# Optimization experiments

Measured on AMD Instinct MI355X. Metric: run time of the kernel, lower is better.

## Reference

```python
import jax, jax.numpy as jnp
import numpy as np


def _conv(x, w, pad):
    return jax.lax.conv_general_dilated(x, w, (1, 1), [(pad, pad), (pad, pad)],
                                        dimension_numbers=('NCHW', 'OIHW', 'NCHW'))


def _cbs(x, w, s, b, pad):
    # Conv + (folded inference BatchNorm as per-channel affine) + SiLU
    y = _conv(x, w, pad) * s[None, :, None, None] + b[None, :, None, None]
    return y * jax.nn.sigmoid(y)


def _pixel_shuffle(x, r):
    N, C, H, W = x.shape
    c = C // (r * r)
    return x.reshape(N, c, r, r, H, W).transpose(0, 1, 4, 2, 5, 3).reshape(N, c, H * r, W * r)


def _pixel_unshuffle(x, r):
    N, C, H, W = x.shape
    h, w = H // r, W // r
    return x.reshape(N, C, h, r, w, r).transpose(0, 1, 3, 5, 2, 4).reshape(N, C * r * r, h, w)


def _carafe(x, dw, db, ew, eb, k, up):
    # Content-aware reassembly: predict per-pixel k*k kernels for up*up sub-positions,
    # softmax-normalize, then gather-multiply-accumulate over k*k neighborhoods.
    N, C, H, W = x.shape
    kt = _conv(x, dw, 0) + db[None, :, None, None]
    if k % 2 == 0:
        kt = jnp.pad(kt, ((0, 0), (0, 0), (k // 2, k // 2 - 1), (k // 2, k // 2 - 1)))
        kt = _conv(kt, ew, 0) + eb[None, :, None, None]
    else:
        kt = _conv(kt, ew, k // 2) + eb[None, :, None, None]
    kt = _pixel_shuffle(kt, up)                     # [N, k*k, H*up, W*up]
    kt = jax.nn.softmax(kt, axis=1)
    # non-overlapping unfold(step=up) -> [N, H, W, k*k, up*up]
    kt = kt.reshape(N, k * k, H, up, W, up).transpose(0, 2, 4, 1, 3, 5).reshape(N, H, W, k * k, up * up)
    if k % 2 == 0:
        xp = jnp.pad(x, ((0, 0), (0, 0), (k // 2, k // 2 - 1), (k // 2, k // 2 - 1)))
    else:
        xp = jnp.pad(x, ((0, 0), (0, 0), (k // 2, k // 2), (k // 2, k // 2)))
    # k*k sliding patches (k is a small static constant)
    patches = jnp.stack([xp[:, :, i:i + H, j:j + W] for i in range(k) for j in range(k)], axis=-1)
    patches = patches.transpose(0, 2, 3, 1, 4)      # [N, H, W, C, k*k]
    out = jnp.einsum('nhwck,nhwkr->nhwcr', patches, kt)  # [N, H, W, C, up*up]
    out = out.reshape(N, H, W, C * up * up).transpose(0, 3, 1, 2)
    return _pixel_shuffle(out, up)


def _forward(x, cv1_w, cv1_s, cv1_b, m1a_w, m1a_s, m1a_b, m1b_w, m1b_s, m1b_b,
             cvm2_w, cvm2_s, cvm2_b, u2_down_w, u2_down_b, u2_enc_w, u2_enc_b,
             m2a_w, m2a_s, m2a_b, m2b_w, m2b_s, m2b_b,
             cvm3_w, cvm3_s, cvm3_b, u3_down_w, u3_down_b, u3_enc_w, u3_enc_b,
             m3a_w, m3a_s, m3a_b, m3b_w, m3b_s, m3b_b, cv2_w, cv2_s, cv2_b):
    C = cv1_w.shape[0] // 2
    t = _cbs(x, cv1_w, cv1_s, cv1_b, 0)
    y, y0 = t[:, :C], t[:, C:]

    def bneck(z, wa, sa, ba, wb, sb, bb):  # shortcut=False, e=1.0
        return _cbs(_cbs(z, wa, sa, ba, 1), wb, sb, bb, 1)

    y1 = bneck(y0, m1a_w, m1a_s, m1a_b, m1b_w, m1b_s, m1b_b)
    y2 = _cbs(_pixel_unshuffle(y1, 2), cvm2_w, cvm2_s, cvm2_b, 0)
    y2 = _carafe(y2, u2_down_w, u2_down_b, u2_enc_w, u2_enc_b, 1, 2) + y1
    y2 = bneck(y2, m2a_w, m2a_s, m2a_b, m2b_w, m2b_s, m2b_b)
    y3 = _cbs(_pixel_unshuffle(y2, 4), cvm3_w, cvm3_s, cvm3_b, 0)
    y3 = _carafe(y3, u3_down_w, u3_down_b, u3_enc_w, u3_enc_b, 2, 4) + y2
    y3 = bneck(y3, m3a_w, m3a_s, m3a_b, m3b_w, m3b_s, m3b_b)
    return _cbs(jnp.concatenate([y, y0, y1, y2, y3], axis=1), cv2_w, cv2_s, cv2_b, 0)


def setup_inputs() -> dict:
    key = jax.random.key(0)
    ks = jax.random.split(key, 16)
    C = 128

    def cbs_p(k, co, ci, ksz):
        k1, k2, k3 = jax.random.split(k, 3)
        w = jax.random.normal(k1, (co, ci, ksz, ksz), jnp.float32) / np.sqrt(ci * ksz * ksz).astype(np.float32)
        s = 1.0 + 0.1 * jax.random.normal(k2, (co,), jnp.float32)
        b = 0.1 * jax.random.normal(k3, (co,), jnp.float32)
        return w, s, b

    d = {}
    d['x'] = jax.random.normal(ks[0], (8, 256, 128, 128), jnp.float32)
    d['cv1_w'], d['cv1_s'], d['cv1_b'] = cbs_p(ks[1], 2 * C, 256, 1)
    for name, kk in (('m1', ks[2]), ('m2', ks[3]), ('m3', ks[4])):
        ka, kb = jax.random.split(kk)
        d[name + 'a_w'], d[name + 'a_s'], d[name + 'a_b'] = cbs_p(ka, C, C, 3)
        d[name + 'b_w'], d[name + 'b_s'], d[name + 'b_b'] = cbs_p(kb, C, C, 3)
    d['cvm2_w'], d['cvm2_s'], d['cvm2_b'] = cbs_p(ks[5], C, 4 * C, 1)
    d['cvm3_w'], d['cvm3_s'], d['cvm3_b'] = cbs_p(ks[6], C, 16 * C, 1)
    d['u2_down_w'] = jax.random.normal(ks[7], (C // 4, C, 1, 1), jnp.float32) / np.sqrt(C).astype(np.float32)
    d['u2_down_b'] = 0.1 * jax.random.normal(ks[8], (C // 4,), jnp.float32)
    d['u2_enc_w'] = jax.random.normal(ks[9], (4, C // 4, 1, 1), jnp.float32) / np.sqrt(C // 4).astype(np.float32)
    d['u2_enc_b'] = 0.1 * jax.random.normal(ks[10], (4,), jnp.float32)
    d['u3_down_w'] = jax.random.normal(ks[11], (C // 4, C, 1, 1), jnp.float32) / np.sqrt(C).astype(np.float32)
    d['u3_down_b'] = 0.1 * jax.random.normal(ks[12], (C // 4,), jnp.float32)
    d['u3_enc_w'] = jax.random.normal(ks[13], (64, C // 4, 2, 2), jnp.float32) / np.sqrt((C // 4) * 4).astype(np.float32)
    d['u3_enc_b'] = 0.1 * jax.random.normal(ks[14], (64,), jnp.float32)
    d['cv2_w'], d['cv2_s'], d['cv2_b'] = cbs_p(ks[15], 256, 5 * C, 1)
    return d


def reference(x, cv1_w, cv1_s, cv1_b, m1a_w, m1a_s, m1a_b, m1b_w, m1b_s, m1b_b,
              cvm2_w, cvm2_s, cvm2_b, u2_down_w, u2_down_b, u2_enc_w, u2_enc_b,
              m2a_w, m2a_s, m2a_b, m2b_w, m2b_s, m2b_b,
              cvm3_w, cvm3_s, cvm3_b, u3_down_w, u3_down_b, u3_enc_w, u3_enc_b,
              m3a_w, m3a_s, m3a_b, m3b_w, m3b_s, m3b_b, cv2_w, cv2_s, cv2_b):
    return _forward(x, cv1_w, cv1_s, cv1_b, m1a_w, m1a_s, m1a_b, m1b_w, m1b_s, m1b_b,
                    cvm2_w, cvm2_s, cvm2_b, u2_down_w, u2_down_b, u2_enc_w, u2_enc_b,
                    m2a_w, m2a_s, m2a_b, m2b_w, m2b_s, m2b_b,
                    cvm3_w, cvm3_s, cvm3_b, u3_down_w, u3_down_b, u3_enc_w, u3_enc_b,
                    m3a_w, m3a_s, m3a_b, m3b_w, m3b_s, m3b_b, cv2_w, cv2_s, cv2_b)
```

## Files before the change

### kernel.cpp

```cpp
#include <hip/hip_runtime.h>

typedef unsigned short u16;
typedef short v8s __attribute__((ext_vector_type(8)));
typedef u16 v8u __attribute__((ext_vector_type(8)));
typedef float v4f __attribute__((ext_vector_type(4)));
typedef __bf16 v8bf __attribute__((ext_vector_type(8)));

__device__ __forceinline__ float bf2f(u16 u) {
    unsigned x = ((unsigned)u) << 16; float f; __builtin_memcpy(&f, &x, 4); return f;
}
__device__ __forceinline__ u16 f2bf(float f) {
    unsigned x; __builtin_memcpy(&x, &f, 4);
    x = x + 0x7FFFu + ((x >> 16) & 1u);
    return (u16)(x >> 16);
}
__device__ __forceinline__ float silu(float v) { return v / (1.f + __expf(-v)); }

__device__ __forceinline__ void gld16(const void* g, void* l) {
    __builtin_amdgcn_global_load_lds(
        (const __attribute__((address_space(1))) unsigned int*)(uintptr_t)g,
        (__attribute__((address_space(3))) unsigned int*)(unsigned int)(uintptr_t)l,
        16, 0, 0);
}

__global__ void cvtw(const float* __restrict__ in, u16* __restrict__ out, int n) {
    int i = blockIdx.x * 256 + threadIdx.x;
    if (i < n) out[i] = f2bf(in[i]);
}
__global__ void wtrans3(const float* __restrict__ in, u16* __restrict__ out) {
    int i = blockIdx.x * 256 + threadIdx.x;
    if (i >= 147456) return;
    int tap = i % 9; int rem = i / 9; int ci = rem & 127; int co = rem >> 7;
    out[((tap * 128 + co) << 7) + ci] = f2bf(in[i]);
}
__global__ void wtrans_ps(const float* __restrict__ in, u16* __restrict__ out, int R2) {
    int i = blockIdx.x * 256 + threadIdx.x;
    int tap = i % R2; int rem = i / R2; int c = rem & 127; int co = rem >> 7;
    out[((tap * 128 + co) << 7) + c] = f2bf(in[i]);
}

__global__ __launch_bounds__(256) void nchw2nhwc(const float* __restrict__ in, u16* __restrict__ out) {
    __shared__ u16 tile[64][72];
    const int n = blockIdx.z, c0 = blockIdx.y * 64, p0 = blockIdx.x * 64;
#pragma unroll
    for (int rep = 0; rep < 16; ++rep) {
        int idx = rep * 256 + threadIdx.x;
        int c = idx >> 6, p = idx & 63;
        tile[c][p] = f2bf(in[((size_t)(n * 256 + c0 + c)) * 16384 + p0 + p]);
    }
    __syncthreads();
#pragma unroll
    for (int rep = 0; rep < 16; ++rep) {
        int idx = rep * 256 + threadIdx.x;
        int p = idx >> 6, c = idx & 63;
        out[((size_t)n * 16384 + p0 + p) * 256 + c0 + c] = tile[c][p];
    }
}

__global__ __launch_bounds__(256, 2) void conv3_mfma(
    const u16* __restrict__ src, int c0, int srcC,
    const u16* __restrict__ wt,
    const float* __restrict__ scale, const float* __restrict__ bias,
    u16* __restrict__ out) {
    __shared__ __align__(16) char smem[49152];
    const int n = blockIdx.y;
    const int hraw = blockIdx.x;
    const int h = ((hraw & 7) << 4) | (hraw >> 3);
    const int tid = threadIdx.x;
    const int lane = tid & 63;
    const int wv = tid >> 6;
    const int r = lane & 15, q = lane >> 4;
    const int wr = wv >> 1, wc = wv & 1;

    v4f acc[4][4];
#pragma unroll
    for (int a = 0; a < 4; ++a)
#pragma unroll
        for (int b = 0; b < 4; ++b) acc[a][b] = (v4f){0.f, 0.f, 0.f, 0.f};

    const size_t rowstride = (size_t)128 * srcC;
    const u16* nbase = src + (size_t)n * 128 * rowstride + c0;

    auto stage = [&](int koff) {
#pragma unroll
        for (int j = 0; j < 12; ++j) {
            int t = wv * 12 + j;
            int kh = t >> 4;
            int hh = h + kh - 1;
            char* dst = smem + t * 1024;
            if ((unsigned)hh < 128u) {
                int px = ((t & 15) << 3) + (lane >> 3);
                int cb = (lane & 7) * 16;
                cb ^= (px & 7) << 4;
                const char* g = (const char*)(nbase + (size_t)hh * rowstride + koff)
                                + (size_t)px * srcC * 2 + cb;
                gld16(g, dst);
            } else {
                *(v8s*)(dst + lane * 16) = (v8s){0, 0, 0, 0, 0, 0, 0, 0};
            }
        }
    };

    auto loadB = [&](v8bf (&B)[12], int kh, int koff, int k0l) {
#pragma unroll
        for (int kw = 0; kw < 3; ++kw)
#pragma unroll
            for (int nt = 0; nt < 4; ++nt)
                B[kw * 4 + nt] = __builtin_bit_cast(v8bf, *(const v8s*)(
                    wt + (size_t)((kh * 3 + kw) * 128 + wc * 64 + nt * 16 + r) * 128
                       + koff + k0l + q * 8));
    };

    auto comp = [&](v8bf (&B)[12], int kh, int k0l) {
#pragma unroll
        for (int kw = 0; kw < 3; ++kw) {
            v8bf afr[4];
#pragma unroll
            for (int mt = 0; mt < 4; ++mt) {
                int p = wr * 64 + mt * 16 + r + kw - 1;
                bool vp = (unsigned)p < 128u;
                int pc = vp ? p : 0;
                int o = kh * 16384 + pc * 128 + k0l * 2 + q * 16;
                o ^= (pc & 7) << 4;
                v8s av = *(const v8s*)(smem + o);
                if (!vp) av = (v8s){0, 0, 0, 0, 0, 0, 0, 0};
                afr[mt] = __builtin_bit_cast(v8bf, av);
            }
#pragma unroll
            for (int mt = 0; mt < 4; ++mt)
#pragma unroll
                for (int nt = 0; nt < 4; ++nt)
                    acc[mt][nt] = __builtin_amdgcn_mfma_f32_16x16x32_bf16(
                        afr[mt], B[kw * 4 + nt], acc[mt][nt], 0, 0, 0);
        }
    };

#pragma unroll
    for (int hf = 0; hf < 2; ++hf) {
        const int koff = hf * 64;
        __syncthreads();
        stage(koff);
        __syncthreads();
#pragma unroll
        for (int k0l = 0; k0l < 64; k0l += 32) {
            v8bf bA[12], bB[12];
            loadB(bA, 0, koff, k0l);
            loadB(bB, 1, koff, k0l);
            comp(bA, 0, k0l);
            loadB(bA, 2, koff, k0l);
            comp(bB, 1, k0l);
            comp(bA, 2, k0l);
        }
    }

    __syncthreads();
    u16* ldsO = (u16*)smem;
#pragma unroll
    for (int nt = 0; nt < 4; ++nt) {
        int co = wc * 64 + nt * 16 + r;
        float s = scale[co], bi = bias[co];
#pragma unroll
        for (int mt = 0; mt < 4; ++mt) {
#pragma unroll
            for (int i = 0; i < 4; ++i) {
                int p = wr * 64 + mt * 16 + q * 4 + i;
                ldsO[p * 136 + co] = f2bf(silu(acc[mt][nt][i] * s + bi));
            }
        }
    }
    __syncthreads();
    const size_t obase = ((size_t)n * 128 + h) * 128;
#pragma unroll
    for (int rep = 0; rep < 8; ++rep) {
        int px = rep * 16 + (tid >> 4);
        int c8 = (tid & 15) * 8;
        *(v8u*)(out + (obase + px) * 128 + c8) = *(const v8u*)&ldsO[px * 136 + c8];
    }
}

__global__ __launch_bounds__(256) void conv1_mfma(
    const u16* __restrict__ src, int srcC,
    const u16* __restrict__ wt,
    const float* __restrict__ scale, const float* __restrict__ bias,
    u16* __restrict__ out, int Cout) {
    __shared__ __align__(16) char smem[34816];
    const int n = blockIdx.z, co0 = blockIdx.y * 128, px0 = blockIdx.x * 128;
    const int tid = threadIdx.x;
    const int lane = tid & 63, wv = tid >> 6;
    const int r = lane & 15, q = lane >> 4;
    const int wr = wv >> 1, wc = wv & 1;

    v4f acc[4][4];
#pragma unroll
    for (int a = 0; a < 4; ++a)
#pragma unroll
        for (int b = 0; b < 4; ++b) acc[a][b] = (v4f){0.f, 0.f, 0.f, 0.f};

    const u16* abase = src + ((size_t)n * 16384 + px0) * srcC;

    auto stage = [&](int buf, int k0) {
#pragma unroll
        for (int j = 0; j < 4; ++j) {
            int o = j * 4096 + tid * 16;
            int s2 = o ^ ((o >> 3) & 0x70);
            int px = s2 >> 7, cb = s2 & 127;
            gld16((const char*)(abase + (size_t)px * srcC + k0) + cb,
                  smem + buf * 16384 + j * 4096 + wv * 1024);
        }
    };
    auto loadB = [&](v8bf (&B)[2][4], int k0) {
        const u16* wrow = wt + (size_t)(co0 + wc * 64 + r) * srcC + k0 + q * 8;
#pragma unroll
        for (int s = 0; s < 2; ++s)
#pragma unroll
            for (int nt = 0; nt < 4; ++nt)
                B[s][nt] = __builtin_bit_cast(v8bf,
                    *(const v8s*)(wrow + s * 32 + (size_t)nt * 16 * srcC));
    };

    v8bf bcur[2][4], bnxt[2][4];
    loadB(bcur, 0);
    stage(0, 0);
    int buf = 0;
    for (int k0 = 0; k0 < srcC; k0 += 64, buf ^= 1) {
        __syncthreads();
        bool more = (k0 + 64 < srcC);
        if (more) {
            loadB(bnxt, k0 + 64);
            stage(buf ^ 1, k0 + 64);
        }
#pragma unroll
        for (int s = 0; s < 2; ++s) {
            v8bf afr[4];
#pragma unroll
            for (int mt = 0; mt < 4; ++mt) {
                int ba = buf * 16384 + (wr * 64 + mt * 16 + r) * 128 + s * 64 + q * 16;
                ba ^= (ba >> 3) & 0x70;
                afr[mt] = __builtin_bit_cast(v8bf, *(const v8s*)(smem + ba));
            }
#pragma unroll
            for (int mt = 0; mt < 4; ++mt)
#pragma unroll
                for (int nt = 0; nt < 4; ++nt)
                    acc[mt][nt] = __builtin_amdgcn_mfma_f32_16x16x32_bf16(
                        afr[mt], bcur[s][nt], acc[mt][nt], 0, 0, 0);
        }
        if (more) {
#pragma unroll
            for (int s = 0; s < 2; ++s)
#pragma unroll
                for (int nt = 0; nt < 4; ++nt) bcur[s][nt] = bnxt[s][nt];
        }
    }

    __syncthreads();
    u16* ldsO = (u16*)smem;
#pragma unroll
    for (int nt = 0; nt < 4; ++nt) {
        int co = co0 + wc * 64 + nt * 16 + r;
        float s = scale[co], bi = bias[co];
#pragma unroll
        for (int mt = 0; mt < 4; ++mt) {
#pragma unroll
            for (int i = 0; i < 4; ++i) {
                int p = wr * 64 + mt * 16 + q * 4 + i;
                ldsO[p * 136 + (wc * 64 + nt * 16 + r)] = f2bf(silu(acc[mt][nt][i] * s + bi));
            }
        }
    }
    __syncthreads();
#pragma unroll
    for (int rep = 0; rep < 8; ++rep) {
        int px = rep * 16 + (tid >> 4);
        int c8 = (tid & 15) * 8;
        *(v8u*)(out + ((size_t)n * 16384 + px0 + px) * Cout + co0 + c8) =
            *(const v8u*)&ldsO[px * 136 + c8];
    }
}

__global__ __launch_bounds__(256) void cat_mfma(
    const u16* __restrict__ s0, const u16* __restrict__ s1,
    const u16* __restrict__ s2, const u16* __restrict__ s3,
    const u16* __restrict__ wt,
    const float* __restrict__ scale, const float* __restrict__ bias,
    float* __restrict__ out) {
    __shared__ __align__(16) u16 lds[2][128][64];
    const int n = blockIdx.z, co0 = blockIdx.y * 128, px0 = blockIdx.x * 128;
    const int tid = threadIdx.x;
    const int lane = tid & 63, wv = tid >> 6;
    const int r = lane & 15, q = lane >> 4;
    const int wr = wv >> 1, wc = wv & 1;

    v4f acc[4][4];
#pragma unroll
    for (int a = 0; a < 4; ++a)
#pragma unroll
        for (int b = 0; b < 4; ++b) acc[a][b] = (v4f){0.f, 0.f, 0.f, 0.f};

    const u16* srcs[4] = {s0, s1, s2, s3};
    const int sCq[4] = {256, 128, 128, 128};
    const int kbq[4] = {0, 256, 384, 512};
    const int segs[10] = {0, 0, 0, 0, 1, 1, 2, 2, 3, 3};
    const int k0s[10] = {0, 64, 128, 192, 0, 64, 0, 64, 0, 64};

    auto stage = [&](int buf, int c) {
        int seg = segs[c]; int sc = sCq[seg]; int k0 = k0s[c];
        const u16* ab = srcs[seg] + ((size_t)n * 16384 + px0) * sc;
#pragma unroll
        for (int j = 0; j < 4; ++j) {
            int o = j * 4096 + tid * 16;
            int s2 = o ^ ((o >> 3) & 0x70);
            int px = s2 >> 7, cb = s2 & 127;
            gld16((const char*)(ab + (size_t)px * sc + k0) + cb,
                  (char*)&lds[buf][0][0] + j * 4096 + wv * 1024);
        }
    };
    auto loadB = [&](v8bf (&B)[2][4], int c) {
        const u16* wrow = wt + (size_t)(co0 + wc * 64 + r) * 640 + kbq[segs[c]] + k0s[c] + q * 8;
#pragma unroll
        for (int s = 0; s < 2; ++s)
#pragma unroll
            for (int nt = 0; nt < 4; ++nt)
                B[s][nt] = __builtin_bit_cast(v8bf,
                    *(const v8s*)(wrow + s * 32 + (size_t)nt * 16 * 640));
    };

    v8bf bcur[2][4], bnxt[2][4];
    loadB(bcur, 0);
    stage(0, 0);
    int buf = 0;
#pragma unroll
    for (int c = 0; c < 10; ++c, buf ^= 1) {
        __syncthreads();
        if (c < 9) {
            loadB(bnxt, c + 1);
            stage(buf ^ 1, c + 1);
        }
#pragma unroll
        for (int s = 0; s < 2; ++s) {
            v8bf afr[4];
#pragma unroll
            for (int mt = 0; mt < 4; ++mt) {
                int ba = (wr * 64 + mt * 16 + r) * 128 + s * 64 + q * 16;
                ba ^= (ba >> 3) & 0x70;
                afr[mt] = __builtin_bit_cast(v8bf,
                    *(const v8s*)((const char*)&lds[buf][0][0] + ba));
            }
#pragma unroll
            for (int mt = 0; mt < 4; ++mt)
#pragma unroll
                for (int nt = 0; nt < 4; ++nt)
                    acc[mt][nt] = __builtin_amdgcn_mfma_f32_16x16x32_bf16(
                        afr[mt], bcur[s][nt], acc[mt][nt], 0, 0, 0);
        }
        if (c < 9) {
#pragma unroll
            for (int s = 0; s < 2; ++s)
#pragma unroll
                for (int nt = 0; nt < 4; ++nt) bcur[s][nt] = bnxt[s][nt];
        }
    }

#pragma unroll
    for (int nt = 0; nt < 4; ++nt) {
        int co = co0 + wc * 64 + nt * 16 + r;
        float s = scale[co], bi = bias[co];
#pragma unroll
        for (int mt = 0; mt < 4; ++mt) {
            int p = px0 + wr * 64 + mt * 16 + q * 4;
            v4f o;
#pragma unroll
            for (int i = 0; i < 4; ++i) o[i] = silu(acc[mt][nt][i] * s + bi);
            *(v4f*)(out + (size_t)(n * 256 + co) * 16384 + p) = o;
        }
    }
}

template <int KH, int KW, int S, int PAD, int CIN>
__global__ __launch_bounds__(256) void conv_mfma(
    const u16* __restrict__ src, int c0, int srcC,
    const u16* __restrict__ wt,
    const float* __restrict__ scale, const float* __restrict__ bias,
    u16* __restrict__ out, int Hin, int Win, int Wout, int Cout) {
    const int n = blockIdx.z;
    const int co0 = blockIdx.y * 64;
    const int hw0 = blockIdx.x * 64;
    const int tid = threadIdx.x;
    const int lane = tid & 63, wv = tid >> 6;
    const int r = lane & 15, q = lane >> 4;
    const int wr = wv >> 1, wc = wv & 1;

    const int m0 = hw0 + wr * 32 + r;
    const int m1 = m0 + 16;
    const int h0 = m0 / Wout, w0 = m0 - h0 * Wout;
    const int h1 = m1 / Wout, w1 = m1 - h1 * Wout;

    v4f acc00 = {0.f, 0.f, 0.f, 0.f}, acc01 = {0.f, 0.f, 0.f, 0.f};
    v4f acc10 = {0.f, 0.f, 0.f, 0.f}, acc11 = {0.f, 0.f, 0.f, 0.f};

    const u16* b0base = wt + (size_t)(co0 + wc * 32 + r) * CIN + q * 8;
    const size_t wtap = (size_t)Cout * CIN;

    int tap = 0;
#pragma unroll
    for (int kh = 0; kh < KH; ++kh)
#pragma unroll
        for (int kw = 0; kw < KW; ++kw, ++tap) {
            int ih0 = h0 * S + kh - PAD, iw0 = w0 * S + kw - PAD;
            int ih1 = h1 * S + kh - PAD, iw1 = w1 * S + kw - PAD;
            bool v0 = ((unsigned)ih0 < (unsigned)Hin) & ((unsigned)iw0 < (unsigned)Win);
            bool v1 = ((unsigned)ih1 < (unsigned)Hin) & ((unsigned)iw1 < (unsigned)Win);
            int p0i = v0 ? (n * Hin + ih0) * Win + iw0 : 0;
            int p1i = v1 ? (n * Hin + ih1) * Win + iw1 : 0;
            const u16* a0 = src + (size_t)p0i * srcC + c0 + q * 8;
            const u16* a1 = src + (size_t)p1i * srcC + c0 + q * 8;
            const u16* b0 = b0base + (size_t)tap * wtap;
            const u16* b1 = b0 + (size_t)16 * CIN;
#pragma unroll
            for (int k = 0; k < CIN; k += 32) {
                v8s za = {0, 0, 0, 0, 0, 0, 0, 0};
                v8s a0s = za, a1s = za;
                if (v0) a0s = *(const v8s*)(a0 + k);
                if (v1) a1s = *(const v8s*)(a1 + k);
                v8s b0s = *(const v8s*)(b0 + k);
                v8s b1s = *(const v8s*)(b1 + k);
                v8bf af0 = __builtin_bit_cast(v8bf, a0s);
                v8bf af1 = __builtin_bit_cast(v8bf, a1s);
                v8bf bw0 = __builtin_bit_cast(v8bf, b0s);
                v8bf bw1 = __builtin_bit_cast(v8bf, b1s);
                acc00 = __builtin_amdgcn_mfma_f32_16x16x32_bf16(af0, bw0, acc00, 0, 0, 0);
                acc01 = __builtin_amdgcn_mfma_f32_16x16x32_bf16(af0, bw1, acc01, 0, 0, 0);
                acc10 = __builtin_amdgcn_mfma_f32_16x16x32_bf16(af1, bw0, acc10, 0, 0, 0);
                acc11 = __builtin_amdgcn_mfma_f32_16x16x32_bf16(af1, bw1, acc11, 0, 0, 0);
            }
        }

    const int HWo = gridDim.x * 64;
#pragma unroll
    for (int ct = 0; ct < 2; ++ct) {
        v4f av0 = ct ? acc01 : acc00;
        v4f av1 = ct ? acc11 : acc10;
        int co = co0 + wc * 32 + ct * 16 + r;
        float s = scale[co], bb = bias[co];
        int mb = hw0 + wr * 32 + q * 4;
#pragma unroll
        for (int i = 0; i < 4; ++i) {
            float x0 = av0[i] * s + bb;
            float x1 = av1[i] * s + bb;
            out[((size_t)n * HWo + mb + i) * Cout + co] = f2bf(silu(x0));
            out[((size_t)n * HWo + mb + 16 + i) * Cout + co] = f2bf(silu(x1));
        }
    }
}

__global__ __launch_bounds__(256) void k_upadd(const u16* __restrict__ y2a,
                                               const u16* __restrict__ y1,
                                               u16* __restrict__ out) {
    int t = blockIdx.x * 256 + threadIdx.x;
    int cg = t & 15; int pix = t >> 4;
    int n = pix >> 14; int p = pix & 16383; int ho = p >> 7; int wo = p & 127;
    const u16* a = y2a + ((size_t)((n * 64 + (ho >> 1)) * 64 + (wo >> 1))) * 128 + cg * 8;
    const u16* b = y1 + (size_t)pix * 128 + cg * 8;
    v8s av = *(const v8s*)a;
    v8s bv = *(const v8s*)b;
    v8u o;
#pragma unroll
    for (int e = 0; e < 8; ++e) o[e] = f2bf(bf2f((u16)av[e]) + bf2f((u16)bv[e]));
    *(v8u*)(out + (size_t)pix * 128 + cg * 8) = o;
}

__global__ __launch_bounds__(256) void k_u3down(const u16* __restrict__ y3a,
                                                const float* __restrict__ w,
                                                const float* __restrict__ b,
                                                float* __restrict__ ktA) {
    int t = blockIdx.x * 256 + threadIdx.x;
    int co = t & 31; int pix = t >> 5;
    const u16* xr = y3a + (size_t)pix * 128;
    const float* wr = w + (size_t)co * 128;
    float acc = b[co];
#pragma unroll 16
    for (int k = 0; k < 128; ++k) acc += bf2f(xr[k]) * wr[k];
    ktA[t] = acc;
}

__global__ __launch_bounds__(256) void k_u3enc(const float* __restrict__ ktA,
                                               const float* __restrict__ ew,
                                               const float* __restrict__ eb,
                                               float* __restrict__ wtsm) {
    int t = blockIdx.x * 256 + threadIdx.x;
    int r = t & 15; int pix = t >> 4;
    int n = pix >> 10; int hw = pix & 1023; int h = hw >> 5; int w = hw & 31;
    float v[4];
#pragma unroll
    for (int kk = 0; kk < 4; ++kk) {
        int co = kk * 16 + r;
        float acc = eb[co];
#pragma unroll
        for (int dh = 0; dh < 2; ++dh)
#pragma unroll
            for (int dw = 0; dw < 2; ++dw) {
                int hh = h - 1 + dh, ww = w - 1 + dw;
                if (hh < 0 || ww < 0) continue;
                const float* kp = ktA + ((size_t)((n * 32 + hh) * 32 + ww)) * 32;
                const float* wp = ew + (size_t)co * 128 + dh * 2 + dw;
                for (int ci = 0; ci < 32; ++ci) acc += kp[ci] * wp[ci * 4];
            }
        v[kk] = acc;
    }
    float mx = fmaxf(fmaxf(v[0], v[1]), fmaxf(v[2], v[3]));
    float e0 = __expf(v[0] - mx), e1 = __expf(v[1] - mx), e2 = __expf(v[2] - mx), e3 = __expf(v[3] - mx);
    float inv = 1.f / (e0 + e1 + e2 + e3);
    float* o = wtsm + (size_t)t * 4;
    o[0] = e0 * inv; o[1] = e1 * inv; o[2] = e2 * inv; o[3] = e3 * inv;
}

__global__ __launch_bounds__(256) void k_carafe(const u16* __restrict__ y3a,
                                                const float* __restrict__ wtsm,
                                                const u16* __restrict__ y2,
                                                u16* __restrict__ out) {
    int t = blockIdx.x * 256 + threadIdx.x;
    int cg = t & 15; int pix = t >> 4;
    int n = pix >> 14; int p = pix & 16383; int ho = p >> 7; int wo = p & 127;
    int h = ho >> 2, i = ho & 3, w = wo >> 2, j = wo & 3, r = i * 4 + j;
    const float* wv = wtsm + ((size_t)((n * 1024 + h * 32 + w) * 16 + r)) * 4;
    v8s yv = *(const v8s*)(y2 + (size_t)pix * 128 + cg * 8);
    float acc[8];
#pragma unroll
    for (int e = 0; e < 8; ++e) acc[e] = bf2f((u16)yv[e]);
#pragma unroll
    for (int kk = 0; kk < 4; ++kk) {
        int ki = kk >> 1, kj = kk & 1;
        int hh = h + ki - 1, ww = w + kj - 1;
        if (hh < 0 || ww < 0) continue;
        float wk = wv[kk];
        v8s sv = *(const v8s*)(y3a + ((size_t)((n * 32 + hh) * 32 + ww)) * 128 + cg * 8);
#pragma unroll
        for (int e = 0; e < 8; ++e) acc[e] += wk * bf2f((u16)sv[e]);
    }
    v8u o;
#pragma unroll
    for (int e = 0; e < 8; ++e) o[e] = f2bf(acc[e]);
    *(v8u*)(out + (size_t)pix * 128 + cg * 8) = o;
}

extern "C" void kernel_launch(void* const* d_in, const int* in_sizes, int n_in,
                              void* d_out, int out_size, void* d_ws, size_t ws_size,
                              hipStream_t stream) {
    const float* x     = (const float*)d_in[0];
    const float* cv1_w = (const float*)d_in[1];
    const float* cv1_s = (const float*)d_in[2];
    const float* cv1_b = (const float*)d_in[3];
    const float* m1a_w = (const float*)d_in[4];
    const float* m1a_s = (const float*)d_in[5];
    const float* m1a_b = (const float*)d_in[6];
    const float* m1b_w = (const float*)d_in[7];
    const float* m1b_s = (const float*)d_in[8];
    const float* m1b_b = (const float*)d_in[9];
    const float* m2a_w = (const float*)d_in[10];
    const float* m2a_s = (const float*)d_in[11];
    const float* m2a_b = (const float*)d_in[12];
    const float* m2b_w = (const float*)d_in[13];
    const float* m2b_s = (const float*)d_in[14];
    const float* m2b_b = (const float*)d_in[15];
    const float* m3a_w = (const float*)d_in[16];
    const float* m3a_s = (const float*)d_in[17];
    const float* m3a_b = (const float*)d_in[18];
    const float* m3b_w = (const float*)d_in[19];
    const float* m3b_s = (const float*)d_in[20];
    const float* m3b_b = (const float*)d_in[21];
    const float* cvm2_w = (const float*)d_in[22];
    const float* cvm2_s = (const float*)d_in[23];
    const float* cvm2_b = (const float*)d_in[24];
    const float* cvm3_w = (const float*)d_in[25];
    const float* cvm3_s = (const float*)d_in[26];
    const float* cvm3_b = (const float*)d_in[27];
    const float* u3_down_w = (const float*)d_in[32];
    const float* u3_down_b = (const float*)d_in[33];
    const float* u3_enc_w  = (const float*)d_in[34];
    const float* u3_enc_b  = (const float*)d_in[35];
    const float* cv2_w = (const float*)d_in[36];
    const float* cv2_s = (const float*)d_in[37];
    const float* cv2_b = (const float*)d_in[38];

    char* ws = (char*)d_ws;
    u16* A    = (u16*)(ws + 0);
    u16* t    = (u16*)(ws + 67108864);
    u16* y1   = (u16*)(ws + 134217728);
    u16* bt   = (u16*)(ws + 167772160);
    u16* te   = (u16*)(ws + 201326592);
    u16* y2a  = (u16*)(ws + 234881024);
    u16* y3a  = (u16*)(ws + 243269632);
    float* ktA = (float*)(ws + 245366784);
    float* wts = (float*)(ws + 246415360);
    u16* w3t  = (u16*)(ws + 248512512);
    u16* wu2  = (u16*)(ws + 250281984);
    u16* wu4  = (u16*)(ws + 250413056);
    u16* wc1  = (u16*)(ws + 250937344);
    u16* wc2  = (u16*)(ws + 251068416);
    u16* y2 = A;
    u16* y3 = A + 16777216;

    dim3 B(256);
    wtrans3<<<576, B, 0, stream>>>(m1a_w, w3t + 0 * 147456);
    wtrans3<<<576, B, 0, stream>>>(m1b_w, w3t + 1 * 147456);
    wtrans3<<<576, B, 0, stream>>>(m2a_w, w3t + 2 * 147456);
    wtrans3<<<576, B, 0, stream>>>(m2b_w, w3t + 3 * 147456);
    wtrans3<<<576, B, 0, stream>>>(m3a_w, w3t + 4 * 147456);
    wtrans3<<<576, B, 0, stream>>>(m3b_w, w3t + 5 * 147456);
    wtrans_ps<<<256, B, 0, stream>>>(cvm2_w, wu2, 4);
    wtrans_ps<<<1024, B, 0, stream>>>(cvm3_w, wu4, 16);
    cvtw<<<256, B, 0, stream>>>(cv1_w, wc1, 65536);
    cvtw<<<640, B, 0, stream>>>(cv2_w, wc2, 163840);

    nchw2nhwc<<<dim3(256, 4, 8), B, 0, stream>>>(x, A);

    conv1_mfma<<<dim3(128, 2, 8), B, 0, stream>>>(A, 256, wc1, cv1_s, cv1_b, t, 256);

    conv3_mfma<<<dim3(128, 8), B, 0, stream>>>(t, 128, 256, w3t + 0 * 147456, m1a_s, m1a_b, bt);
    conv3_mfma<<<dim3(128, 8), B, 0, stream>>>(bt, 0, 128, w3t + 1 * 147456, m1b_s, m1b_b, y1);

    conv_mfma<2, 2, 2, 0, 128><<<dim3(64, 2, 8), B, 0, stream>>>(
        y1, 0, 128, wu2, cvm2_s, cvm2_b, y2a, 128, 128, 64, 128);

    k_upadd<<<8192, B, 0, stream>>>(y2a, y1, te);

    conv3_mfma<<<dim3(128, 8), B, 0, stream>>>(te, 0, 128, w3t + 2 * 147456, m2a_s, m2a_b, bt);
    conv3_mfma<<<dim3(128, 8), B, 0, stream>>>(bt, 0, 128, w3t + 3 * 147456, m2b_s, m2b_b, y2);

    conv_mfma<4, 4, 4, 0, 128><<<dim3(16, 2, 8), B, 0, stream>>>(
        y2, 0, 128, wu4, cvm3_s, cvm3_b, y3a, 128, 128, 32, 128);

    k_u3down<<<1024, B, 0, stream>>>(y3a, u3_down_w, u3_down_b, ktA);
    k_u3enc<<<512, B, 0, stream>>>(ktA, u3_enc_w, u3_enc_b, wts);
    k_carafe<<<8192, B, 0, stream>>>(y3a, wts, y2, te);

    conv3_mfma<<<dim3(128, 8), B, 0, stream>>>(te, 0, 128, w3t + 4 * 147456, m3a_s, m3a_b, bt);
    conv3_mfma<<<dim3(128, 8), B, 0, stream>>>(bt, 0, 128, w3t + 5 * 147456, m3b_s, m3b_b, y3);

    cat_mfma<<<dim3(128, 2, 8), B, 0, stream>>>(t, y1, y2, y3, wc2, cv2_s, cv2_b, (float*)d_out);
}
```

Before: 1.388 ms.

## Split conv3 output channels across blocks and double-buffer input staging

The 3x3 conv kernel now has each block compute 64 output channels instead of 128, which doubles the grid to 256x8. Its K loop becomes four 32-channel chunks with double-buffered LDS staging, so the global-to-LDS loads for the next chunk overlap the MFMA work on the current one. Fewer accumulators allow launch bounds of 3 blocks per CU, raising occupancy. The cost is that each block re-stages the same input rows for both channel halves, and more weight fragments are held in registers per chunk.

```diff
diff --git a/kernel.cpp b/kernel.cpp
--- a/kernel.cpp
+++ b/kernel.cpp
@@ -57,124 +57,112 @@
     }
 }
 
-__global__ __launch_bounds__(256, 2) void conv3_mfma(
+__global__ __launch_bounds__(256, 3) void conv3_mfma(
     const u16* __restrict__ src, int c0, int srcC,
     const u16* __restrict__ wt,
     const float* __restrict__ scale, const float* __restrict__ bias,
     u16* __restrict__ out) {
     __shared__ __align__(16) char smem[49152];
-    const int n = blockIdx.y;
-    const int hraw = blockIdx.x;
-    const int h = ((hraw & 7) << 4) | (hraw >> 3);
+    const int bx = blockIdx.x, n = blockIdx.y;
+    const int h = ((bx & 7) << 4) | (bx >> 4);
+    const int co0 = ((bx >> 3) & 1) * 64;
     const int tid = threadIdx.x;
-    const int lane = tid & 63;
-    const int wv = tid >> 6;
+    const int lane = tid & 63, wv = tid >> 6;
     const int r = lane & 15, q = lane >> 4;
     const int wr = wv >> 1, wc = wv & 1;
 
-    v4f acc[4][4];
+    v4f acc[4][2];
 #pragma unroll
     for (int a = 0; a < 4; ++a)
 #pragma unroll
-        for (int b = 0; b < 4; ++b) acc[a][b] = (v4f){0.f, 0.f, 0.f, 0.f};
+        for (int b = 0; b < 2; ++b) acc[a][b] = (v4f){0.f, 0.f, 0.f, 0.f};
 
     const size_t rowstride = (size_t)128 * srcC;
     const u16* nbase = src + (size_t)n * 128 * rowstride + c0;
 
-    auto stage = [&](int koff) {
-#pragma unroll
-        for (int j = 0; j < 12; ++j) {
-            int t = wv * 12 + j;
-            int kh = t >> 4;
+    auto stage = [&](int buf, int k0) {
+#pragma unroll
+        for (int j = 0; j < 6; ++j) {
+            int t = wv * 6 + j;
+            int kh = t >> 3;
             int hh = h + kh - 1;
-            char* dst = smem + t * 1024;
+            char* dst = smem + buf * 24576 + t * 1024;
             if ((unsigned)hh < 128u) {
-                int px = ((t & 15) << 3) + (lane >> 3);
-                int cb = (lane & 7) * 16;
-                cb ^= (px & 7) << 4;
-                const char* g = (const char*)(nbase + (size_t)hh * rowstride + koff)
-                                + (size_t)px * srcC * 2 + cb;
-                gld16(g, dst);
+                int l = ((t & 7) << 10) + lane * 16;
+                int sw = l ^ ((l >> 3) & 0x70);
+                int px = sw >> 6, cb = sw & 63;
+                gld16((const char*)(nbase + (size_t)hh * rowstride + k0)
+                          + (size_t)px * srcC * 2 + cb,
+                      dst);
             } else {
                 *(v8s*)(dst + lane * 16) = (v8s){0, 0, 0, 0, 0, 0, 0, 0};
             }
         }
     };
 
-    auto loadB = [&](v8bf (&B)[12], int kh, int koff, int k0l) {
-#pragma unroll
-        for (int kw = 0; kw < 3; ++kw)
-#pragma unroll
-            for (int nt = 0; nt < 4; ++nt)
-                B[kw * 4 + nt] = __builtin_bit_cast(v8bf, *(const v8s*)(
-                    wt + (size_t)((kh * 3 + kw) * 128 + wc * 64 + nt * 16 + r) * 128
-                       + koff + k0l + q * 8));
-    };
-
-    auto comp = [&](v8bf (&B)[12], int kh, int k0l) {
-#pragma unroll
-        for (int kw = 0; kw < 3; ++kw) {
-            v8bf afr[4];
+    stage(0, 0);
+    int buf = 0;
+#pragma unroll
+    for (int ch = 0; ch < 4; ++ch, buf ^= 1) {
+        const int k0 = ch * 32;
+        __syncthreads();
+
+        v8bf bfr[9][2];
+#pragma unroll
+        for (int tap = 0; tap < 9; ++tap)
+#pragma unroll
+            for (int nt = 0; nt < 2; ++nt)
+                bfr[tap][nt] = __builtin_bit_cast(v8bf, *(const v8s*)(
+                    wt + (size_t)((tap * 128 + co0 + wc * 32 + nt * 16 + r) << 7)
+                       + k0 + q * 8));
+
+        if (ch < 3) stage(buf ^ 1, k0 + 32);
+
+        const char* abase = smem + buf * 24576;
+#pragma unroll
+        for (int tap = 0; tap < 9; ++tap) {
+            const int kh = tap / 3, kw = tap % 3;
 #pragma unroll
             for (int mt = 0; mt < 4; ++mt) {
                 int p = wr * 64 + mt * 16 + r + kw - 1;
                 bool vp = (unsigned)p < 128u;
                 int pc = vp ? p : 0;
-                int o = kh * 16384 + pc * 128 + k0l * 2 + q * 16;
-                o ^= (pc & 7) << 4;
-                v8s av = *(const v8s*)(smem + o);
+                int b = (pc << 6) + q * 16;
+                b ^= (b >> 3) & 0x70;
+                v8s av = *(const v8s*)(abase + (kh << 13) + b);
                 if (!vp) av = (v8s){0, 0, 0, 0, 0, 0, 0, 0};
-                afr[mt] = __builtin_bit_cast(v8bf, av);
-            }
-#pragma unroll
-            for (int mt = 0; mt < 4; ++mt)
-#pragma unroll
-                for (int nt = 0; nt < 4; ++nt)
+                v8bf af = __builtin_bit_cast(v8bf, av);
+#pragma unroll
+                for (int nt = 0; nt < 2; ++nt)
                     acc[mt][nt] = __builtin_amdgcn_mfma_f32_16x16x32_bf16(
-                        afr[mt], B[kw * 4 + nt], acc[mt][nt], 0, 0, 0);
-        }
-    };
-
-#pragma unroll
-    for (int hf = 0; hf < 2; ++hf) {
-        const int koff = hf * 64;
-        __syncthreads();
-        stage(koff);
-        __syncthreads();
-#pragma unroll
-        for (int k0l = 0; k0l < 64; k0l += 32) {
-            v8bf bA[12], bB[12];
-            loadB(bA, 0, koff, k0l);
-            loadB(bB, 1, koff, k0l);
-            comp(bA, 0, k0l);
-            loadB(bA, 2, koff, k0l);
-            comp(bB, 1, k0l);
-            comp(bA, 2, k0l);
+                        af, bfr[tap][nt], acc[mt][nt], 0, 0, 0);
+            }
         }
     }
 
     __syncthreads();
     u16* ldsO = (u16*)smem;
 #pragma unroll
-    for (int nt = 0; nt < 4; ++nt) {
-        int co = wc * 64 + nt * 16 + r;
+    for (int nt = 0; nt < 2; ++nt) {
+        int coL = wc * 32 + nt * 16 + r;
+        int co = co0 + coL;
         float s = scale[co], bi = bias[co];
 #pragma unroll
         for (int mt = 0; mt < 4; ++mt) {
 #pragma unroll
             for (int i = 0; i < 4; ++i) {
                 int p = wr * 64 + mt * 16 + q * 4 + i;
-                ldsO[p * 136 + co] = f2bf(silu(acc[mt][nt][i] * s + bi));
+                ldsO[p * 72 + coL] = f2bf(silu(acc[mt][nt][i] * s + bi));
             }
         }
     }
     __syncthreads();
     const size_t obase = ((size_t)n * 128 + h) * 128;
 #pragma unroll
-    for (int rep = 0; rep < 8; ++rep) {
-        int px = rep * 16 + (tid >> 4);
-        int c8 = (tid & 15) * 8;
-        *(v8u*)(out + (obase + px) * 128 + c8) = *(const v8u*)&ldsO[px * 136 + c8];
+    for (int rep = 0; rep < 4; ++rep) {
+        int px = rep * 32 + (tid >> 3);
+        int c8 = (tid & 7) * 8;
+        *(v8u*)(out + (obase + px) * 128 + co0 + c8) = *(const v8u*)&ldsO[px * 72 + c8];
     }
 }
 
@@ -616,16 +604,16 @@
 
     conv1_mfma<<<dim3(128, 2, 8), B, 0, stream>>>(A, 256, wc1, cv1_s, cv1_b, t, 256);
 
-    conv3_mfma<<<dim3(128, 8), B, 0, stream>>>(t, 128, 256, w3t + 0 * 147456, m1a_s, m1a_b, bt);
-    conv3_mfma<<<dim3(128, 8), B, 0, stream>>>(bt, 0, 128, w3t + 1 * 147456, m1b_s, m1b_b, y1);
+    conv3_mfma<<<dim3(256, 8), B, 0, stream>>>(t, 128, 256, w3t + 0 * 147456, m1a_s, m1a_b, bt);
+    conv3_mfma<<<dim3(256, 8), B, 0, stream>>>(bt, 0, 128, w3t + 1 * 147456, m1b_s, m1b_b, y1);
 
     conv_mfma<2, 2, 2, 0, 128><<<dim3(64, 2, 8), B, 0, stream>>>(
         y1, 0, 128, wu2, cvm2_s, cvm2_b, y2a, 128, 128, 64, 128);
 
     k_upadd<<<8192, B, 0, stream>>>(y2a, y1, te);
 
-    conv3_mfma<<<dim3(128, 8), B, 0, stream>>>(te, 0, 128, w3t + 2 * 147456, m2a_s, m2a_b, bt);
-    conv3_mfma<<<dim3(128, 8), B, 0, stream>>>(bt, 0, 128, w3t + 3 * 147456, m2b_s, m2b_b, y2);
+    conv3_mfma<<<dim3(256, 8), B, 0, stream>>>(te, 0, 128, w3t + 2 * 147456, m2a_s, m2a_b, bt);
+    conv3_mfma<<<dim3(256, 8), B, 0, stream>>>(bt, 0, 128, w3t + 3 * 147456, m2b_s, m2b_b, y2);
 
     conv_mfma<4, 4, 4, 0, 128><<<dim3(16, 2, 8), B, 0, stream>>>(
         y2, 0, 128, wu4, cvm3_s, cvm3_b, y3a, 128, 128, 32, 128);
@@ -634,8 +622,8 @@
     k_u3enc<<<512, B, 0, stream>>>(ktA, u3_enc_w, u3_enc_b, wts);
     k_carafe<<<8192, B, 0, stream>>>(y3a, wts, y2, te);
 
-    conv3_mfma<<<dim3(128, 8), B, 0, stream>>>(te, 0, 128, w3t + 4 * 147456, m3a_s, m3a_b, bt);
-    conv3_mfma<<<dim3(128, 8), B, 0, stream>>>(bt, 0, 128, w3t + 5 * 147456, m3b_s, m3b_b, y3);
+    conv3_mfma<<<dim3(256, 8), B, 0, stream>>>(te, 0, 128, w3t + 4 * 147456, m3a_s, m3a_b, bt);
+    conv3_mfma<<<dim3(256, 8), B, 0, stream>>>(bt, 0, 128, w3t + 5 * 147456, m3b_s, m3b_b, y3);
 
     cat_mfma<<<dim3(128, 2, 8), B, 0, stream>>>(t, y1, y2, y3, wc2, cv2_s, cv2_b, (float*)d_out);
 }
```

New measurement: 1.377 ms. No clear change (-0.8%).
